# Performance work log

Hardware: AMD Instinct MI355X
Metric: run time of the kernel (lower is better)

The kernel has to match this reference:

```python
import jax, jax.numpy as jnp
import numpy as np

LAN_DIM = 2048
FEA_DIM = 128
N = 65536
SHRINK_THRES = 0.0025
R = 1.0
EPS = 1e-12


def setup_inputs() -> dict:
    key = jax.random.key(0)
    k1, k2 = jax.random.split(key)
    x = jax.random.normal(k1, (N, FEA_DIM), dtype=jnp.float32)
    # reset_parameters: uniform(-stdv, stdv), stdv = 1/sqrt(fea_dim)
    stdv = 1.0 / np.sqrt(FEA_DIM)
    weight = jax.random.uniform(k2, (LAN_DIM, FEA_DIM), dtype=jnp.float32,
                                minval=-stdv, maxval=stdv)
    return {"input": x, "weight": weight}


def reference(input, weight):
    x = input                                    # [N, D]
    logits = jnp.einsum('nd,ld->nl', x, weight)  # [N, L]
    att = jax.nn.softmax(logits, axis=1)
    # hard_shrink_relu
    shifted = att - SHRINK_THRES
    att = jax.nn.relu(shifted) * att / (jnp.abs(shifted) + EPS)
    # F.normalize(p=1, dim=1): x / max(||x||_1, eps); att is nonneg
    att = att / jnp.maximum(jnp.sum(att, axis=1, keepdims=True), EPS)
    output = jnp.einsum('nl,ld->nd', att, weight)  # [N, D]

    # nearest landmark: argmax over att per sample
    ind = jnp.argmax(att, axis=1)                # [N]
    nl = weight[ind]                             # [N, D]
    # second-nearest: overwrite each row's argmax entry with the row min, re-argmax
    row_min = jnp.min(att, axis=1)               # [N]
    att2 = att.at[jnp.arange(N), ind].set(row_min)
    ind2 = jnp.argmax(att2, axis=1)
    nl2 = weight[ind2]                           # [N, D]

    # center of codebook, samples within radius R (boolean mask instead of
    # data-dependent-length index list, for jit compatibility)
    cen = jnp.mean(weight, axis=0)               # [D]
    dist = jnp.sqrt(jnp.sum((x - cen[None, :]) ** 2, axis=1))
    col = dist < R                               # [N] bool

    return output, att, nl, nl2, col
```

## Files before the change

kernel.cpp:

```cpp
#include <hip/hip_runtime.h>
#include <math.h>

#define NS 65536
#define LAN 2048
#define FEA 128

constexpr float THRES = 0.0025f;
constexpr float FEPS  = 1e-12f;
constexpr int BM   = 32;
constexpr int MAXS = 63;

typedef _Float16 half8 __attribute__((ext_vector_type(8)));
typedef float    f32x4 __attribute__((ext_vector_type(4)));

__global__ void k_prep(const float* __restrict__ W,
                       _Float16* __restrict__ Wh, _Float16* __restrict__ Wl,
                       float* __restrict__ censum) {
    if (blockIdx.x < 1024) {
        int i = blockIdx.x * 256 + threadIdx.x;
        float w = W[i];
        _Float16 h = (_Float16)w;
        Wh[i] = h;
        Wl[i] = (_Float16)(w - (float)h);
    } else {
        __shared__ f32x4 sred[8][32];
        const int b = blockIdx.x - 1024;
        const int tid = threadIdx.x;
        const int rg = tid >> 5, q = tid & 31;
        const f32x4* W4 = (const f32x4*)W;
        f32x4 p = (f32x4){0.f, 0.f, 0.f, 0.f};
        #pragma unroll
        for (int j = 0; j < 8; ++j) {
            int row = b * 64 + rg * 8 + j;
            p += W4[(size_t)row * 32 + q];
        }
        sred[rg][q] = p;
        __syncthreads();
        if (tid < 32) {
            f32x4 s = sred[0][tid];
            #pragma unroll
            for (int w = 1; w < 8; ++w) s += sred[w][tid];
            #pragma unroll
            for (int e = 0; e < 4; ++e)
                atomicAdd(&censum[tid * 4 + e], s[e]);
        }
    }
}

__device__ static inline void gload_lds16(const void* g, void* l) {
    __builtin_amdgcn_global_load_lds(
        (const __attribute__((address_space(1))) void*)g,
        (__attribute__((address_space(3))) void*)l, 16, 0, 0);
}

#define RAWBAR() { asm volatile("s_waitcnt lgkmcnt(0)" ::: "memory"); \
                   __builtin_amdgcn_s_barrier(); \
                   __builtin_amdgcn_sched_barrier(0); }

__global__ __launch_bounds__(512, 2) void k_main(
    const float* __restrict__ X, const float* __restrict__ W,
    const _Float16* __restrict__ Wh, const _Float16* __restrict__ Wl,
    const float* __restrict__ censum,
    float* __restrict__ o_out, float* __restrict__ o_att,
    float* __restrict__ o_nl, float* __restrict__ o_nl2,
    float* __restrict__ o_col)
{
    __shared__ __align__(16) char s_pool[147456];
    __shared__ float s_red[8][BM];
    __shared__ float s_rsinv[BM], s_Sinv[BM];
    __shared__ int   s_ind[BM], s_ind2[BM], s_cnt[BM];

    const int tid  = threadIdx.x;
    const int wv   = tid >> 6;
    const int lane = tid & 63;
    const int g    = lane >> 4;
    const int m    = lane & 15;
    const int row0 = blockIdx.x * BM;
    constexpr int XOFF = 131072;

    #define ISSUE_BH(t_, buf_)                                                      \
        {                                                                           \
            const char* gh_ = (const char*)(Wh + (size_t)(wv * 256 + (t_) * 16) * FEA); \
            char* lb_ = s_pool + (buf_) * 65536 + wv * 8192;                        \
            _Pragma("unroll")                                                       \
            for (int i_ = 0; i_ < 4; ++i_) {                                        \
                int c_ = i_ * 64 + lane;                                            \
                int gc_ = c_ ^ ((c_ >> 4) & 7);                                     \
                gload_lds16(gh_ + gc_ * 16, lb_ + i_ * 1024);                       \
            }                                                                       \
        }
    #define ISSUE_BL(t_, buf_)                                                      \
        {                                                                           \
            const char* gl_ = (const char*)(Wl + (size_t)(wv * 256 + (t_) * 16) * FEA); \
            char* lb_ = s_pool + (buf_) * 65536 + wv * 8192 + 4096;                 \
            _Pragma("unroll")                                                       \
            for (int i_ = 0; i_ < 4; ++i_) {                                        \
                int c_ = i_ * 64 + lane;                                            \
                int gc_ = c_ ^ ((c_ >> 4) & 7);                                     \
                gload_lds16(gl_ + gc_ * 16, lb_ + i_ * 1024);                       \
            }                                                                       \
        }

    {
        const char* xg = (const char*)(X + (size_t)row0 * FEA);
        gload_lds16(xg + (wv * 2 + 0) * 1024 + lane * 16, s_pool + XOFF + (wv * 2 + 0) * 1024);
        gload_lds16(xg + (wv * 2 + 1) * 1024 + lane * 16, s_pool + XOFF + (wv * 2 + 1) * 1024);
    }
    ISSUE_BH(0, 0) ISSUE_BL(0, 0)
    ISSUE_BH(1, 1) ISSUE_BL(1, 1)
    asm volatile("s_waitcnt vmcnt(16)" ::: "memory");
    __builtin_amdgcn_s_barrier();
    __builtin_amdgcn_sched_barrier(0);

    half8 afh[2][4], afl[2][4];
    #pragma unroll
    for (int rt = 0; rt < 2; ++rt)
        #pragma unroll
        for (int kb = 0; kb < 4; ++kb) {
            const char* base = s_pool + XOFF + (rt * 16 + m) * 512 + (kb * 8 + g * 2) * 16;
            f32x4 xa = *(const f32x4*)(base);
            f32x4 xb = *(const f32x4*)(base + 16);
            half8 h, l;
            #pragma unroll
            for (int e = 0; e < 4; ++e) {
                _Float16 hh = (_Float16)xa[e];
                h[e] = hh; l[e] = (_Float16)(xa[e] - (float)hh);
            }
            #pragma unroll
            for (int e = 0; e < 4; ++e) {
                _Float16 hh = (_Float16)xb[e];
                h[4 + e] = hh; l[4 + e] = (_Float16)(xb[e] - (float)hh);
            }
            afh[rt][kb] = h; afl[rt][kb] = l;
        }

    const float inv2048 = 1.0f / 2048.0f;
    #pragma unroll
    for (int u = 0; u < 4; ++u) {
        const int lr = wv * 4 + u;
        float2 x2 = *(const float2*)(s_pool + XOFF + lr * 512 + lane * 8);
        float dx0 = x2.x - censum[lane * 2] * inv2048;
        float dx1 = x2.y - censum[lane * 2 + 1] * inv2048;
        float dd = dx0 * dx0 + dx1 * dx1;
        #pragma unroll
        for (int off = 32; off >= 1; off >>= 1) dd += __shfl_xor(dd, off);
        if (lane == 0) o_col[row0 + lr] = (sqrtf(dd) < 1.0f) ? 1.0f : 0.0f;
    }

    f32x4 acc[2][16];
    #pragma unroll
    for (int rt = 0; rt < 2; ++rt)
        #pragma unroll
        for (int t = 0; t < 16; ++t) acc[rt][t] = (f32x4){0.f, 0.f, 0.f, 0.f};
    float ssum[2][4];
    #pragma unroll
    for (int rt = 0; rt < 2; ++rt)
        #pragma unroll
        for (int r = 0; r < 4; ++r) ssum[rt][r] = 0.f;

    #pragma unroll 16
    for (int t = 0; t < 16; ++t) {
        const int buf = t & 1;
        const char* bb = s_pool + buf * 65536 + wv * 8192;
        if (t <= 14) { asm volatile("s_waitcnt vmcnt(12)" ::: "memory"); }
        else         { asm volatile("s_waitcnt vmcnt(4)"  ::: "memory"); }
        __builtin_amdgcn_sched_barrier(0);
        half8 bh[4];
        #pragma unroll
        for (int kb = 0; kb < 4; ++kb) {
            int off = (m * 256 + kb * 64 + g * 16) ^ ((m & 7) << 4);
            bh[kb] = *(const half8*)(bb + off);
        }
        asm volatile("s_waitcnt lgkmcnt(0)" ::: "memory");
        __builtin_amdgcn_sched_barrier(0);
        if (t < 14) ISSUE_BH(t + 2, buf)
        __builtin_amdgcn_s_setprio(1);
        #pragma unroll
        for (int kb = 0; kb < 4; ++kb)
            #pragma unroll
            for (int rt = 0; rt < 2; ++rt) {
                acc[rt][t] = __builtin_amdgcn_mfma_f32_16x16x32_f16(afh[rt][kb], bh[kb], acc[rt][t], 0, 0, 0);
                acc[rt][t] = __builtin_amdgcn_mfma_f32_16x16x32_f16(afl[rt][kb], bh[kb], acc[rt][t], 0, 0, 0);
            }
        __builtin_amdgcn_s_setprio(0);
        if (t <= 13)      { asm volatile("s_waitcnt vmcnt(12)" ::: "memory"); }
        else if (t == 14) { asm volatile("s_waitcnt vmcnt(8)"  ::: "memory"); }
        else              { asm volatile("s_waitcnt vmcnt(0)"  ::: "memory"); }
        __builtin_amdgcn_sched_barrier(0);
        half8 bl[4];
        #pragma unroll
        for (int kb = 0; kb < 4; ++kb) {
            int off = (m * 256 + kb * 64 + g * 16) ^ ((m & 7) << 4);
            bl[kb] = *(const half8*)(bb + 4096 + off);
        }
        asm volatile("s_waitcnt lgkmcnt(0)" ::: "memory");
        __builtin_amdgcn_sched_barrier(0);
        if (t < 14) ISSUE_BL(t + 2, buf)
        __builtin_amdgcn_s_setprio(1);
        #pragma unroll
        for (int kb = 0; kb < 4; ++kb)
            #pragma unroll
            for (int rt = 0; rt < 2; ++rt)
                acc[rt][t] = __builtin_amdgcn_mfma_f32_16x16x32_f16(afh[rt][kb], bl[kb], acc[rt][t], 0, 0, 0);
        __builtin_amdgcn_s_setprio(0);
        #pragma unroll
        for (int rt = 0; rt < 2; ++rt)
            #pragma unroll
            for (int r = 0; r < 4; ++r) {
                float e = __expf(acc[rt][t][r]);
                acc[rt][t][r] = e;
                ssum[rt][r] += e;
            }
    }
    #undef ISSUE_BH
    #undef ISSUE_BL


    #pragma unroll
    for (int rt = 0; rt < 2; ++rt)
        #pragma unroll
        for (int r = 0; r < 4; ++r) {
            float s = ssum[rt][r];
            #pragma unroll
            for (int off = 8; off >= 1; off >>= 1) s += __shfl_xor(s, off);
            if (m == 0) s_red[wv][rt*16 + g*4 + r] = s;
        }
    __syncthreads();
    if (tid < BM) {
        float s = s_red[0][tid];
        #pragma unroll
        for (int w = 1; w < 8; ++w) s += s_red[w][tid];
        s_rsinv[tid] = 1.0f / s;
        s_cnt[tid] = 0;
    }
    __syncthreads();

    int*   s_scol = (int*)s_pool;
    float* s_sval = (float*)(s_pool + 16384);
    #pragma unroll
    for (int rt = 0; rt < 2; ++rt)
        #pragma unroll
        for (int r = 0; r < 4; ++r) {
            const int lr = rt*16 + g*4 + r;
            const float ri = s_rsinv[lr];
            float S = 0.f;
            #pragma unroll
            for (int t = 0; t < 16; ++t) {
                float soft = acc[rt][t][r] * ri;
                float sh = soft - THRES;
                if (sh > 0.f) {
                    float v = sh * soft / (sh + FEPS);
                    S += v;
                    int p = atomicAdd(&s_cnt[lr], 1);
                    if (p < MAXS) { s_scol[lr*64 + p] = wv*256 + t*16 + m; s_sval[lr*64 + p] = v; }
                }
            }
            #pragma unroll
            for (int off = 8; off >= 1; off >>= 1) S += __shfl_xor(S, off);
            if (m == 0) s_red[wv][lr] = S;
        }
    __syncthreads();
    if (tid < BM) {
        float S = s_red[0][tid];
        #pragma unroll
        for (int w = 1; w < 8; ++w) S += s_red[w][tid];
        s_Sinv[tid] = 1.0f / fmaxf(S, FEPS);
        const int cn = min(s_cnt[tid], MAXS);
        float t1v = -1.f, t2v = -1.f; int t1c = 0x7fffffff, t2c = 0x7fffffff;
        for (int p = 0; p < cn; ++p) {
            float v = s_sval[tid*64 + p]; int c = s_scol[tid*64 + p];
            if (v > t1v || (v == t1v && c < t1c)) {
                t2v = t1v; t2c = t1c; t1v = v; t1c = c;
            } else if (v > t2v || (v == t2v && c < t2c)) {
                t2v = v; t2c = c;
            }
        }
        s_ind[tid]  = (cn >= 1) ? t1c : 0;
        s_ind2[tid] = (cn >= 2) ? t2c : 0;
    }
    __syncthreads();

    #pragma unroll
    for (int u = 0; u < 4; ++u) {
        const int lr = wv*4 + u;
        const int grow = row0 + lr;
        const int d0 = lane * 2;
        const int cnt = min(s_cnt[lr], MAXS);
        const float si = s_Sinv[lr];
        float o0 = 0.f, o1 = 0.f;
        for (int s2 = 0; s2 < cnt; ++s2) {
            const int c = s_scol[lr*64 + s2];
            const float v = s_sval[lr*64 + s2];
            const float2 w2 = *(const float2*)(W + (size_t)c * FEA + d0);
            o0 += v * w2.x; o1 += v * w2.y;
        }
        *(float2*)(o_out + (size_t)grow * FEA + d0) = make_float2(o0 * si, o1 * si);
        const int i1 = s_ind[lr], i2 = s_ind2[lr];
        *(float2*)(o_nl  + (size_t)grow * FEA + d0) = *(const float2*)(W + (size_t)i1 * FEA + d0);
        *(float2*)(o_nl2 + (size_t)grow * FEA + d0) = *(const float2*)(W + (size_t)i2 * FEA + d0);
    }

    float* comp  = (float*)(s_pool + 32768);
    f32x4* comp4 = (f32x4*)comp;
    const f32x4 fz4 = (f32x4){0.f, 0.f, 0.f, 0.f};
    #pragma unroll
    for (int ph = 0; ph < 4; ++ph) {
        #pragma unroll
        for (int e = 0; e < 8; ++e) comp4[e * 512 + tid] = fz4;
        RAWBAR();
        {
            const int lr = ph * 8 + wv;
            const int cn = min(s_cnt[lr], MAXS);
            const float si = s_Sinv[lr];
            for (int p = lane; p < cn; p += 64)
                comp[(wv << 11) + s_scol[lr*64 + p]] = s_sval[lr*64 + p] * si;
        }
        RAWBAR();
        float* gdst = o_att + (size_t)(row0 + ph * 8) * LAN;
        #pragma unroll
        for (int e = 0; e < 8; ++e) {
            int fi = e * 512 + tid;
            __builtin_nontemporal_store(comp4[fi], (f32x4*)gdst + fi);
        }
        RAWBAR();
    }
}

extern "C" void kernel_launch(void* const* d_in, const int* in_sizes, int n_in,
                              void* d_out, int out_size, void* d_ws, size_t ws_size,
                              hipStream_t stream) {
    const float* X = (const float*)d_in[0];
    const float* W = (const float*)d_in[1];

    _Float16* Wh = (_Float16*)d_ws;
    _Float16* Wl = Wh + (size_t)LAN * FEA;
    float*    censum = (float*)(Wl + (size_t)LAN * FEA);

    float* out      = (float*)d_out;
    float* o_output = out;
    float* o_att    = o_output + (size_t)NS * FEA;
    float* o_nl     = o_att    + (size_t)NS * LAN;
    float* o_nl2    = o_nl     + (size_t)NS * FEA;
    float* o_col    = o_nl2    + (size_t)NS * FEA;

    hipMemsetAsync(censum, 0, FEA * sizeof(float), stream);
    k_prep<<<1056, 256, 0, stream>>>(W, Wh, Wl, censum);
    k_main<<<NS / BM, 512, 0, stream>>>(X, W, Wh, Wl, censum,
                                        o_output, o_att, o_nl, o_nl2, o_col);
}
```

Measured before the change: 296.0 us.

## Overlap att zero-fill stores with the GEMM loop and scatter nonzeros afterwards

The dense zero-fill of the 32x2048 attention tile moves out of the epilogue and into the main MFMA loop. Each iteration issues nontemporal zero stores for two rows, so the output write traffic overlaps with compute, and the vmcnt waits are retuned to count these extra outstanding stores. The epilogue then scatters only the surviving sparse values directly to global memory. This drops the LDS staging and the three barriers per phase. The risks are correctness: the sparse scatter must land after the zero stores to the same addresses, and the vmcnt counts must stay exact so weight loads are not consumed early.

```diff
diff --git a/kernel.cpp b/kernel.cpp
--- a/kernel.cpp
+++ b/kernel.cpp
@@ -53,10 +53,6 @@
         (__attribute__((address_space(3))) void*)l, 16, 0, 0);
 }
 
-#define RAWBAR() { asm volatile("s_waitcnt lgkmcnt(0)" ::: "memory"); \
-                   __builtin_amdgcn_s_barrier(); \
-                   __builtin_amdgcn_sched_barrier(0); }
-
 __global__ __launch_bounds__(512, 2) void k_main(
     const float* __restrict__ X, const float* __restrict__ W,
     const _Float16* __restrict__ Wh, const _Float16* __restrict__ Wl,
@@ -77,6 +73,7 @@
     const int m    = lane & 15;
     const int row0 = blockIdx.x * BM;
     constexpr int XOFF = 131072;
+    const f32x4 fz4 = (f32x4){0.f, 0.f, 0.f, 0.f};
 
     #define ISSUE_BH(t_, buf_)                                                      \
         {                                                                           \
@@ -162,8 +159,10 @@
     for (int t = 0; t < 16; ++t) {
         const int buf = t & 1;
         const char* bb = s_pool + buf * 65536 + wv * 8192;
-        if (t <= 14) { asm volatile("s_waitcnt vmcnt(12)" ::: "memory"); }
-        else         { asm volatile("s_waitcnt vmcnt(4)"  ::: "memory"); }
+        if (t == 0)       { asm volatile("s_waitcnt vmcnt(12)" ::: "memory"); }
+        else if (t == 1)  { asm volatile("s_waitcnt vmcnt(14)" ::: "memory"); }
+        else if (t <= 14) { asm volatile("s_waitcnt vmcnt(16)" ::: "memory"); }
+        else              { asm volatile("s_waitcnt vmcnt(8)"  ::: "memory"); }
         __builtin_amdgcn_sched_barrier(0);
         half8 bh[4];
         #pragma unroll
@@ -183,9 +182,11 @@
                 acc[rt][t] = __builtin_amdgcn_mfma_f32_16x16x32_f16(afl[rt][kb], bh[kb], acc[rt][t], 0, 0, 0);
             }
         __builtin_amdgcn_s_setprio(0);
-        if (t <= 13)      { asm volatile("s_waitcnt vmcnt(12)" ::: "memory"); }
-        else if (t == 14) { asm volatile("s_waitcnt vmcnt(8)"  ::: "memory"); }
-        else              { asm volatile("s_waitcnt vmcnt(0)"  ::: "memory"); }
+        if (t == 0)       { asm volatile("s_waitcnt vmcnt(12)" ::: "memory"); }
+        else if (t == 1)  { asm volatile("s_waitcnt vmcnt(14)" ::: "memory"); }
+        else if (t <= 13) { asm volatile("s_waitcnt vmcnt(16)" ::: "memory"); }
+        else if (t == 14) { asm volatile("s_waitcnt vmcnt(12)" ::: "memory"); }
+        else              { asm volatile("s_waitcnt vmcnt(4)"  ::: "memory"); }
         __builtin_amdgcn_sched_barrier(0);
         half8 bl[4];
         #pragma unroll
@@ -211,6 +212,12 @@
                 acc[rt][t][r] = e;
                 ssum[rt][r] += e;
             }
+        {
+            const int zr = 2 * t + (tid >> 8);
+            float* zdst = o_att + (size_t)(row0 + zr) * LAN + (size_t)(tid & 255) * 4;
+            __builtin_nontemporal_store(fz4, (f32x4*)zdst);
+            __builtin_nontemporal_store(fz4, (f32x4*)zdst + 256);
+        }
     }
     #undef ISSUE_BH
     #undef ISSUE_BL
@@ -300,29 +307,13 @@
         *(float2*)(o_nl2 + (size_t)grow * FEA + d0) = *(const float2*)(W + (size_t)i2 * FEA + d0);
     }
 
-    float* comp  = (float*)(s_pool + 32768);
-    f32x4* comp4 = (f32x4*)comp;
-    const f32x4 fz4 = (f32x4){0.f, 0.f, 0.f, 0.f};
-    #pragma unroll
-    for (int ph = 0; ph < 4; ++ph) {
-        #pragma unroll
-        for (int e = 0; e < 8; ++e) comp4[e * 512 + tid] = fz4;
-        RAWBAR();
-        {
-            const int lr = ph * 8 + wv;
-            const int cn = min(s_cnt[lr], MAXS);
-            const float si = s_Sinv[lr];
-            for (int p = lane; p < cn; p += 64)
-                comp[(wv << 11) + s_scol[lr*64 + p]] = s_sval[lr*64 + p] * si;
-        }
-        RAWBAR();
-        float* gdst = o_att + (size_t)(row0 + ph * 8) * LAN;
-        #pragma unroll
-        for (int e = 0; e < 8; ++e) {
-            int fi = e * 512 + tid;
-            __builtin_nontemporal_store(comp4[fi], (f32x4*)gdst + fi);
-        }
-        RAWBAR();
+    {
+        const int lrp = tid >> 4, j = tid & 15;
+        const int cn = min(s_cnt[lrp], MAXS);
+        const float si = s_Sinv[lrp];
+        float* rbase = o_att + (size_t)(row0 + lrp) * LAN;
+        for (int p = j; p < cn; p += 16)
+            __builtin_nontemporal_store(s_sval[lrp*64 + p] * si, rbase + s_scol[lrp*64 + p]);
     }
 }
 
```

Result: faster. 263.7 us, median of 2 (-10.9%).
